# Kernel tuning notes

Hardware: AMD Instinct MI355X
Metric: run time of the kernel (lower is better)

The kernel has to match this reference:

```python
import jax, jax.numpy as jnp
import numpy as np

N, H, V, K = 2048, 1024, 50304, 16
C = V // K  # tokens per POS cluster


def setup_inputs() -> dict:
    key = jax.random.key(0)
    kx, ky, kw, kl = jax.random.split(key, 4)
    x = jax.random.normal(kx, (N, H), dtype=jnp.float32)
    y = jax.random.randint(ky, (N,), 0, V, dtype=jnp.int32)
    # consistent POS label: token y belongs to cluster y // C
    y_pos = (y // C).astype(jnp.int32)
    # pos2token[i] = token ids of cluster i (equal contiguous partition)
    pos2token = jnp.arange(V, dtype=jnp.int32).reshape(K, C)
    # token_in_pos_id[i][v] = within-cluster index of token v in cluster i
    token_in_pos_id = jnp.broadcast_to(jnp.arange(V, dtype=jnp.int32) % C, (K, V))
    cluster_w = jax.random.normal(kw, (H, K), dtype=jnp.float32) * 0.02
    logits = jax.random.normal(kl, (H, V), dtype=jnp.float32) * 0.02
    return {"x": x, "y": y, "y_pos": y_pos, "pos2token": pos2token,
            "token_in_pos_id": token_in_pos_id, "cluster_w": cluster_w, "logits": logits}


def reference(x, y, y_pos, pos2token, token_in_pos_id, cluster_w, logits):
    # cluster (POS) log-probs: [N, K]
    cluster_ll = jax.nn.log_softmax(x @ cluster_w, axis=1)
    # per-cluster weight slices gathered once: [H, K, C]
    W = logits[:, pos2token.reshape(-1)].reshape(H, K, C)
    # tail logits for every token against every cluster's token set: [N, K, C]
    tail_lp = jax.nn.log_softmax(jnp.einsum('nh,hkc->nkc', x, W), axis=-1)
    n = jnp.arange(y.shape[0])
    within = token_in_pos_id[y_pos, y]          # within-cluster target id
    nll = -cluster_ll[n, y_pos] - tail_lp[n, y_pos, within]
    return nll
```

## Files before the change

kernel.cpp:

```cpp
#include <hip/hip_runtime.h>
#include <hip/hip_bf16.h>

#define NROW 2048
#define HDIM 1024
#define VOC  50304
#define KCL  16
#define CDIM 3144

#define MT 128
#define NT 128
#define BK 32
#define CAP 256

#define WS_SUMEXP 0
#define WS_COUNTS 2048
#define WS_PART   2064
#define WS_ZTGT   4112
#define WS_TCOL   6160
#define WS_ROWS   8208
#define WS_XG     40976

typedef __attribute__((ext_vector_type(8))) short short8;
typedef __attribute__((ext_vector_type(4))) short short4v;
typedef __attribute__((ext_vector_type(4))) float f32x4;

__device__ __forceinline__ ushort2 f2bf2(float a, float b) {
    union { __hip_bfloat162 h; ushort2 u; } cv;
    cv.h = __float22bfloat162_rn(float2{a, b});
    return cv.u;
}

__device__ __forceinline__ void gload_lds16(const void* g, void* l) {
    const uint32_t __attribute__((address_space(1)))* gp =
        reinterpret_cast<const uint32_t __attribute__((address_space(1)))*>(
            reinterpret_cast<uintptr_t>(g));
    uint32_t __attribute__((address_space(3)))* lp =
        reinterpret_cast<uint32_t __attribute__((address_space(3)))*>(
            static_cast<uint32_t>(reinterpret_cast<uintptr_t>(l)));
    __builtin_amdgcn_global_load_lds(gp, lp, 16, 0, 0);
}

__global__ void scatter_kernel(const int* __restrict__ y,
                               const int* __restrict__ y_pos,
                               const int* __restrict__ tip,
                               int* ws_i) {
    int n = blockIdx.x * 256 + threadIdx.x;
    if (n >= NROW) return;
    int kn = y_pos[n];
    int slot = atomicAdd(&ws_i[WS_COUNTS + kn], 1);
    ws_i[WS_ROWS + kn * NROW + slot] = n;
    ws_i[WS_TCOL + n] = tip[kn * VOC + y[n]];
}

__global__ void prep_kernel(const float* __restrict__ x,
                            const float* __restrict__ cw,
                            const int* __restrict__ ws_i, float* ws_f) {
    const int wave = threadIdx.x >> 6;
    const int lane = threadIdx.x & 63;
    const int gw = blockIdx.x * 4 + wave;
    const int k = gw >> 8;
    const int slot = gw & (CAP - 1);
    const int Mk = ws_i[WS_COUNTS + k];
    short4v* dst = (short4v*)((const short*)(ws_i + WS_XG) + ((size_t)gw << 10));
    if (slot >= Mk) {
        short4v z = {0, 0, 0, 0};
#pragma unroll
        for (int q = 0; q < 4; q++) dst[q * 64 + lane] = z;
        return;
    }
    const int n = ws_i[WS_ROWS + k * NROW + slot];
    const float4* xr = (const float4*)(x + (size_t)n * HDIM);
    float4 v[4];
#pragma unroll
    for (int q = 0; q < 4; q++) v[q] = xr[q * 64 + lane];
#pragma unroll
    for (int q = 0; q < 4; q++) {
        union { ushort2 u2[2]; short4v s4; } t;
        t.u2[0] = f2bf2(v[q].x, v[q].y);
        t.u2[1] = f2bf2(v[q].z, v[q].w);
        dst[q * 64 + lane] = t.s4;
    }
    float acc[KCL];
#pragma unroll
    for (int kk = 0; kk < KCL; kk++) acc[kk] = 0.f;
#pragma unroll
    for (int q = 0; q < 4; q++) {
        const float* vf = (const float*)&v[q];
#pragma unroll
        for (int e = 0; e < 4; e++) {
            const int h = q * 256 + lane * 4 + e;
            const float xv = vf[e];
            const float4* cwr = (const float4*)(cw + (size_t)h * KCL);
#pragma unroll
            for (int qq = 0; qq < 4; qq++) {
                float4 w = cwr[qq];
                acc[qq * 4 + 0] += xv * w.x;
                acc[qq * 4 + 1] += xv * w.y;
                acc[qq * 4 + 2] += xv * w.z;
                acc[qq * 4 + 3] += xv * w.w;
            }
        }
    }
#pragma unroll
    for (int off = 32; off >= 1; off >>= 1) {
#pragma unroll
        for (int kk = 0; kk < KCL; kk++) acc[kk] += __shfl_down(acc[kk], off);
    }
    if (lane == 0) {
        float m = acc[0];
#pragma unroll
        for (int kk = 1; kk < KCL; kk++) m = fmaxf(m, acc[kk]);
        float s = 0.f;
#pragma unroll
        for (int kk = 0; kk < KCL; kk++) s += __expf(acc[kk] - m);
        ws_f[WS_PART + n] = (m + __logf(s)) - acc[k];
    }
}

__launch_bounds__(256, 2)
__global__ void tail_kernel(const float* __restrict__ logits,
                            const int* ws_i, float* ws_f) {
    __shared__ __align__(16) short As[4 * MT * 8];
    __shared__ __align__(16) short Bs[4 * NT * 8];
    __shared__ int   lrow[MT];
    __shared__ int   ltcol[MT];
    __shared__ float rowsum[MT];

    const int k  = blockIdx.y;
    const int ct = blockIdx.x;
    const int rt = blockIdx.z;
    const int Mk = ws_i[WS_COUNTS + k];
    if (rt * MT >= Mk) return;

    const int tid = threadIdx.x;
    if (tid < MT) {
        int r = rt * MT + tid;
        int rid = (r < Mk) ? ws_i[WS_ROWS + k * NROW + r] : -1;
        lrow[tid]  = rid;
        ltcol[tid] = (rid >= 0) ? ws_i[WS_TCOL + rid] : -1;
        rowsum[tid] = 0.f;
    }

    const short* xg = (const short*)(ws_i + WS_XG)
                    + ((size_t)(k * CAP + rt * MT) << 10);
    const int row0 = tid & 127;
    const int k80  = tid >> 7;
    const short* xrow = xg + (size_t)row0 * HDIM;

    const int w  = tid >> 6;
    const int l  = tid & 63;
    const int col0 = ct * NT + 2 * l;
    const int cp   = (col0 <= CDIM - 2) ? col0 : (CDIM - 2);
    const float* bp = logits + (size_t)(w * 8) * VOC + (k * CDIM + cp);

    const int wr   = (w >> 1) * 64;
    const int wc   = (w & 1) * 64;
    const int quad = l >> 4;
    const int lm   = l & 15;

    f32x4 acc[4][4];
#pragma unroll
    for (int mi = 0; mi < 4; mi++)
#pragma unroll
        for (int ni = 0; ni < 4; ni++) acc[mi][ni] = (f32x4)(0.f);

    __syncthreads();

    for (int h0 = 0; h0 < HDIM; h0 += BK) {
        gload_lds16(xrow + (k80 * 8) + h0,       &As[(size_t)tid * 8]);
        gload_lds16(xrow + ((k80 + 2) * 8) + h0, &As[(size_t)(256 + tid) * 8]);

        {
            float2 bv[8];
            const float* bpp = bp + (size_t)h0 * VOC;
#pragma unroll
            for (int j = 0; j < 8; j++)
                bv[j] = *(const float2*)(bpp + (size_t)j * VOC);
            union { ushort2 u2[4]; short8 s8; } ue, uo;
#pragma unroll
            for (int t = 0; t < 4; t++) {
                ue.u2[t] = f2bf2(bv[2 * t].x, bv[2 * t + 1].x);
                uo.u2[t] = f2bf2(bv[2 * t].y, bv[2 * t + 1].y);
            }
            *(short8*)&Bs[(size_t)(w * 128 + l) * 8]      = ue.s8;
            *(short8*)&Bs[(size_t)(w * 128 + 64 + l) * 8] = uo.s8;
        }
        __syncthreads();

        short8 a[4], b[4];
#pragma unroll
        for (int mi = 0; mi < 4; mi++)
            a[mi] = *(const short8*)&As[(size_t)(quad * 128 + wr + mi * 16 + lm) * 8];
#pragma unroll
        for (int ni = 0; ni < 4; ni++) {
            int C = wc + ni * 16 + lm;
            int cperm = (C >> 1) | ((C & 1) << 6);
            b[ni] = *(const short8*)&Bs[(size_t)(quad * 128 + cperm) * 8];
        }
#pragma unroll
        for (int mi = 0; mi < 4; mi++)
#pragma unroll
            for (int ni = 0; ni < 4; ni++)
                acc[mi][ni] = __builtin_amdgcn_mfma_f32_16x16x32_bf16(
                    a[mi], b[ni], acc[mi][ni], 0, 0, 0);
        __syncthreads();
    }

#pragma unroll
    for (int mi = 0; mi < 4; mi++) {
#pragma unroll
        for (int r = 0; r < 4; r++) {
            int row_local = wr + mi * 16 + quad * 4 + r;
            int rid = lrow[row_local];
            int tc  = ltcol[row_local];
            float s = 0.f;
#pragma unroll
            for (int ni = 0; ni < 4; ni++) {
                int cl = ct * NT + wc + ni * 16 + lm;
                float z = acc[mi][ni][r];
                if (rid >= 0 && cl < CDIM) {
                    s += __expf(z);
                    if (cl == tc) ws_f[WS_ZTGT + rid] = z;
                }
            }
            s += __shfl_xor(s, 1);
            s += __shfl_xor(s, 2);
            s += __shfl_xor(s, 4);
            s += __shfl_xor(s, 8);
            if (lm == 0 && rid >= 0) atomicAdd(&rowsum[row_local], s);
        }
    }
    __syncthreads();
    if (tid < MT) {
        int rid = lrow[tid];
        if (rid >= 0) atomicAdd(&ws_f[WS_SUMEXP + rid], rowsum[tid]);
    }
}

__global__ void finalize_kernel(const float* ws_f, float* __restrict__ out) {
    int n = blockIdx.x * 256 + threadIdx.x;
    if (n >= NROW) return;
    out[n] = ws_f[WS_PART + n] + __logf(ws_f[WS_SUMEXP + n]) - ws_f[WS_ZTGT + n];
}

extern "C" void kernel_launch(void* const* d_in, const int* in_sizes, int n_in,
                              void* d_out, int out_size, void* d_ws, size_t ws_size,
                              hipStream_t stream) {
    const float* x      = (const float*)d_in[0];
    const int*   y      = (const int*)d_in[1];
    const int*   y_pos  = (const int*)d_in[2];
    const int*   tip    = (const int*)d_in[4];
    const float* cw     = (const float*)d_in[5];
    const float* logits = (const float*)d_in[6];
    float* out  = (float*)d_out;
    float* ws_f = (float*)d_ws;
    int*   ws_i = (int*)d_ws;

    hipMemsetAsync(d_ws, 0, (size_t)(NROW + KCL) * 4, stream);

    scatter_kernel<<<NROW / 256, 256, 0, stream>>>(y, y_pos, tip, ws_i);
    prep_kernel<<<KCL * CAP / 4, 256, 0, stream>>>(x, cw, ws_i, ws_f);

    dim3 grid((CDIM + NT - 1) / NT, KCL, CAP / MT);
    tail_kernel<<<grid, 256, 0, stream>>>(logits, ws_i, ws_f);

    finalize_kernel<<<NROW / 256, 256, 0, stream>>>(ws_f, out);
}
```

Before: 383.8 us.

## Double-buffer tail GEMM, shrink column tile, and pre-transpose gathered x layout

The tail GEMM now double-buffers its A and B LDS tiles, issuing the next K-slice's global loads before the current MFMAs so load latency overlaps compute. The column tile drops from 128 to 64 with an occupancy hint of 4 blocks per CU. The prep kernel stages bf16 x rows in shared memory and writes them in an h-major blocked layout so tail loads are contiguous per K-step. The trade-off is more LDS per block, fewer MFMAs per B load, and B column reads that are now only 4-byte scalars.

```diff
diff --git a/kernel.cpp b/kernel.cpp
--- a/kernel.cpp
+++ b/kernel.cpp
@@ -8,9 +8,12 @@
 #define CDIM 3144
 
 #define MT 128
-#define NT 128
+#define NTC 64
 #define BK 32
 #define CAP 256
+
+#define ASZ (4 * 128 * 8)
+#define BSZ (4 * 64 * 8)
 
 #define WS_SUMEXP 0
 #define WS_COUNTS 2048
@@ -55,73 +58,87 @@
 __global__ void prep_kernel(const float* __restrict__ x,
                             const float* __restrict__ cw,
                             const int* __restrict__ ws_i, float* ws_f) {
-    const int wave = threadIdx.x >> 6;
+    __shared__ __align__(16) short rb[4][128][8];
+
+    const int wv   = threadIdx.x >> 6;
     const int lane = threadIdx.x & 63;
-    const int gw = blockIdx.x * 4 + wave;
-    const int k = gw >> 8;
-    const int slot = gw & (CAP - 1);
+    const int b = blockIdx.x;
+    const int k = b >> 6;
+    const int slot0 = (b & 63) * 4;
+    const int slot  = slot0 + wv;
     const int Mk = ws_i[WS_COUNTS + k];
-    short4v* dst = (short4v*)((const short*)(ws_i + WS_XG) + ((size_t)gw << 10));
-    if (slot >= Mk) {
-        short4v z = {0, 0, 0, 0};
-#pragma unroll
-        for (int q = 0; q < 4; q++) dst[q * 64 + lane] = z;
-        return;
-    }
-    const int n = ws_i[WS_ROWS + k * NROW + slot];
-    const float4* xr = (const float4*)(x + (size_t)n * HDIM);
+
     float4 v[4];
-#pragma unroll
-    for (int q = 0; q < 4; q++) v[q] = xr[q * 64 + lane];
+    if (slot < Mk) {
+        const int n = ws_i[WS_ROWS + k * NROW + slot];
+        const float4* xr = (const float4*)(x + (size_t)n * HDIM);
+#pragma unroll
+        for (int q = 0; q < 4; q++) v[q] = xr[q * 64 + lane];
+    } else {
+#pragma unroll
+        for (int q = 0; q < 4; q++) v[q] = float4{0.f, 0.f, 0.f, 0.f};
+    }
 #pragma unroll
     for (int q = 0; q < 4; q++) {
-        union { ushort2 u2[2]; short4v s4; } t;
+        union { ushort2 u2[2]; uint2 u; } t;
         t.u2[0] = f2bf2(v[q].x, v[q].y);
         t.u2[1] = f2bf2(v[q].z, v[q].w);
-        dst[q * 64 + lane] = t.s4;
-    }
-    float acc[KCL];
-#pragma unroll
-    for (int kk = 0; kk < KCL; kk++) acc[kk] = 0.f;
-#pragma unroll
-    for (int q = 0; q < 4; q++) {
-        const float* vf = (const float*)&v[q];
-#pragma unroll
-        for (int e = 0; e < 4; e++) {
-            const int h = q * 256 + lane * 4 + e;
-            const float xv = vf[e];
-            const float4* cwr = (const float4*)(cw + (size_t)h * KCL);
-#pragma unroll
-            for (int qq = 0; qq < 4; qq++) {
-                float4 w = cwr[qq];
-                acc[qq * 4 + 0] += xv * w.x;
-                acc[qq * 4 + 1] += xv * w.y;
-                acc[qq * 4 + 2] += xv * w.z;
-                acc[qq * 4 + 3] += xv * w.w;
+        *(uint2*)&rb[wv][q * 32 + (lane >> 1)][(lane & 1) * 4] = t.u;
+    }
+    if (slot < Mk) {
+        float acc[KCL];
+#pragma unroll
+        for (int kk = 0; kk < KCL; kk++) acc[kk] = 0.f;
+#pragma unroll
+        for (int q = 0; q < 4; q++) {
+            const float* vf = (const float*)&v[q];
+#pragma unroll
+            for (int e = 0; e < 4; e++) {
+                const int h = q * 256 + lane * 4 + e;
+                const float xv = vf[e];
+                const float4* cwr = (const float4*)(cw + (size_t)h * KCL);
+#pragma unroll
+                for (int qq = 0; qq < 4; qq++) {
+                    float4 wgt = cwr[qq];
+                    acc[qq * 4 + 0] += xv * wgt.x;
+                    acc[qq * 4 + 1] += xv * wgt.y;
+                    acc[qq * 4 + 2] += xv * wgt.z;
+                    acc[qq * 4 + 3] += xv * wgt.w;
+                }
             }
         }
-    }
-#pragma unroll
-    for (int off = 32; off >= 1; off >>= 1) {
-#pragma unroll
-        for (int kk = 0; kk < KCL; kk++) acc[kk] += __shfl_down(acc[kk], off);
-    }
-    if (lane == 0) {
-        float m = acc[0];
-#pragma unroll
-        for (int kk = 1; kk < KCL; kk++) m = fmaxf(m, acc[kk]);
-        float s = 0.f;
-#pragma unroll
-        for (int kk = 0; kk < KCL; kk++) s += __expf(acc[kk] - m);
-        ws_f[WS_PART + n] = (m + __logf(s)) - acc[k];
-    }
-}
-
-__launch_bounds__(256, 2)
+#pragma unroll
+        for (int off = 32; off >= 1; off >>= 1) {
+#pragma unroll
+            for (int kk = 0; kk < KCL; kk++) acc[kk] += __shfl_down(acc[kk], off);
+        }
+        if (lane == 0) {
+            const int n = ws_i[WS_ROWS + k * NROW + slot];
+            float m = acc[0];
+#pragma unroll
+            for (int kk = 1; kk < KCL; kk++) m = fmaxf(m, acc[kk]);
+            float s = 0.f;
+#pragma unroll
+            for (int kk = 0; kk < KCL; kk++) s += __expf(acc[kk] - m);
+            ws_f[WS_PART + n] = (m + __logf(s)) - acc[k];
+        }
+    }
+    __syncthreads();
+    {
+        const int h8 = threadIdx.x >> 1;
+        const int sp = (threadIdx.x & 1) * 2;
+        short* o = (short*)(ws_i + WS_XG)
+                 + ((size_t)k * (128 * 256) + (size_t)h8 * 256 + slot0 + sp) * 8;
+        *(short8*)(o)     = *(const short8*)&rb[sp][h8][0];
+        *(short8*)(o + 8) = *(const short8*)&rb[sp + 1][h8][0];
+    }
+}
+
+__launch_bounds__(256, 4)
 __global__ void tail_kernel(const float* __restrict__ logits,
                             const int* ws_i, float* ws_f) {
-    __shared__ __align__(16) short As[4 * MT * 8];
-    __shared__ __align__(16) short Bs[4 * NT * 8];
+    __shared__ __align__(16) short As[2 * ASZ];
+    __shared__ __align__(16) short Bs[2 * BSZ];
     __shared__ int   lrow[MT];
     __shared__ int   ltcol[MT];
     __shared__ float rowsum[MT];
@@ -141,68 +158,77 @@
         rowsum[tid] = 0.f;
     }
 
-    const short* xg = (const short*)(ws_i + WS_XG)
-                    + ((size_t)(k * CAP + rt * MT) << 10);
+    const short* xgT = (const short*)(ws_i + WS_XG);
     const int row0 = tid & 127;
     const int k80  = tid >> 7;
-    const short* xrow = xg + (size_t)row0 * HDIM;
-
-    const int w  = tid >> 6;
-    const int l  = tid & 63;
-    const int col0 = ct * NT + 2 * l;
-    const int cp   = (col0 <= CDIM - 2) ? col0 : (CDIM - 2);
-    const float* bp = logits + (size_t)(w * 8) * VOC + (k * CDIM + cp);
-
-    const int wr   = (w >> 1) * 64;
-    const int wc   = (w & 1) * 64;
-    const int quad = l >> 4;
-    const int lm   = l & 15;
-
-    f32x4 acc[4][4];
+    const short* aSrc0 = xgT + ((size_t)k * (128 * 256)
+                              + (size_t)(k80 * 256 + rt * MT + row0)) * 8;
+    const short* aSrc1 = aSrc0 + 2 * 256 * 8;
+
+    const int c  = tid & 63;
+    const int kg = tid >> 6;
+    const int col0 = ct * NTC + c;
+    const int cp = (col0 < CDIM) ? col0 : (CDIM - 1);
+    const float* bSrc = logits + (size_t)(kg * 8) * VOC + ((size_t)k * CDIM + cp);
+
+    const int w  = tid >> 6, l = tid & 63;
+    const int wr = (w & 1) * 64;
+    const int wc = (w >> 1) * 32;
+    const int quad = l >> 4, lm = l & 15;
+
+    f32x4 acc[4][2];
 #pragma unroll
     for (int mi = 0; mi < 4; mi++)
 #pragma unroll
-        for (int ni = 0; ni < 4; ni++) acc[mi][ni] = (f32x4)(0.f);
-
+        for (int ni = 0; ni < 2; ni++) acc[mi][ni] = (f32x4)(0.f);
+
+    gload_lds16(aSrc0, As + tid * 8);
+    gload_lds16(aSrc1, As + (256 + tid) * 8);
+    {
+        float bv[8];
+#pragma unroll
+        for (int j = 0; j < 8; j++) bv[j] = bSrc[(size_t)j * VOC];
+        union { ushort2 u2[4]; short8 s8; } u;
+#pragma unroll
+        for (int jj = 0; jj < 4; jj++) u.u2[jj] = f2bf2(bv[2 * jj], bv[2 * jj + 1]);
+        *(short8*)(Bs + (kg * 64 + c) * 8) = u.s8;
+    }
     __syncthreads();
 
-    for (int h0 = 0; h0 < HDIM; h0 += BK) {
-        gload_lds16(xrow + (k80 * 8) + h0,       &As[(size_t)tid * 8]);
-        gload_lds16(xrow + ((k80 + 2) * 8) + h0, &As[(size_t)(256 + tid) * 8]);
-
-        {
-            float2 bv[8];
-            const float* bpp = bp + (size_t)h0 * VOC;
+    for (int t = 0; t < HDIM / BK; ++t) {
+        const int cur = t & 1;
+        short* asb = As + cur * ASZ;
+        short* bsb = Bs + cur * BSZ;
+        float bv[8];
+        const bool pf = (t < HDIM / BK - 1);
+        if (pf) {
+            short* asn = As + (cur ^ 1) * ASZ;
+            gload_lds16(aSrc0 + (size_t)(t + 1) * 8192, asn + tid * 8);
+            gload_lds16(aSrc1 + (size_t)(t + 1) * 8192, asn + (256 + tid) * 8);
 #pragma unroll
             for (int j = 0; j < 8; j++)
-                bv[j] = *(const float2*)(bpp + (size_t)j * VOC);
-            union { ushort2 u2[4]; short8 s8; } ue, uo;
-#pragma unroll
-            for (int t = 0; t < 4; t++) {
-                ue.u2[t] = f2bf2(bv[2 * t].x, bv[2 * t + 1].x);
-                uo.u2[t] = f2bf2(bv[2 * t].y, bv[2 * t + 1].y);
-            }
-            *(short8*)&Bs[(size_t)(w * 128 + l) * 8]      = ue.s8;
-            *(short8*)&Bs[(size_t)(w * 128 + 64 + l) * 8] = uo.s8;
-        }
-        __syncthreads();
-
-        short8 a[4], b[4];
+                bv[j] = bSrc[(size_t)((t + 1) * BK + j) * VOC];
+        }
+        short8 a[4], b[2];
 #pragma unroll
         for (int mi = 0; mi < 4; mi++)
-            a[mi] = *(const short8*)&As[(size_t)(quad * 128 + wr + mi * 16 + lm) * 8];
-#pragma unroll
-        for (int ni = 0; ni < 4; ni++) {
-            int C = wc + ni * 16 + lm;
-            int cperm = (C >> 1) | ((C & 1) << 6);
-            b[ni] = *(const short8*)&Bs[(size_t)(quad * 128 + cperm) * 8];
-        }
+            a[mi] = *(const short8*)(asb + (quad * 128 + wr + mi * 16 + lm) * 8);
+#pragma unroll
+        for (int ni = 0; ni < 2; ni++)
+            b[ni] = *(const short8*)(bsb + (quad * 64 + wc + ni * 16 + lm) * 8);
 #pragma unroll
         for (int mi = 0; mi < 4; mi++)
 #pragma unroll
-            for (int ni = 0; ni < 4; ni++)
+            for (int ni = 0; ni < 2; ni++)
                 acc[mi][ni] = __builtin_amdgcn_mfma_f32_16x16x32_bf16(
                     a[mi], b[ni], acc[mi][ni], 0, 0, 0);
+        if (pf) {
+            short* bsn = Bs + (cur ^ 1) * BSZ;
+            union { ushort2 u2[4]; short8 s8; } u;
+#pragma unroll
+            for (int jj = 0; jj < 4; jj++) u.u2[jj] = f2bf2(bv[2 * jj], bv[2 * jj + 1]);
+            *(short8*)(bsn + (kg * 64 + c) * 8) = u.s8;
+        }
         __syncthreads();
     }
 
@@ -215,8 +241,8 @@
             int tc  = ltcol[row_local];
             float s = 0.f;
 #pragma unroll
-            for (int ni = 0; ni < 4; ni++) {
-                int cl = ct * NT + wc + ni * 16 + lm;
+            for (int ni = 0; ni < 2; ni++) {
+                int cl = ct * NTC + wc + ni * 16 + lm;
                 float z = acc[mi][ni][r];
                 if (rid >= 0 && cl < CDIM) {
                     s += __expf(z);
@@ -261,7 +287,7 @@
     scatter_kernel<<<NROW / 256, 256, 0, stream>>>(y, y_pos, tip, ws_i);
     prep_kernel<<<KCL * CAP / 4, 256, 0, stream>>>(x, cw, ws_i, ws_f);
 
-    dim3 grid((CDIM + NT - 1) / NT, KCL, CAP / MT);
+    dim3 grid((CDIM + NTC - 1) / NTC, KCL, CAP / MT);
     tail_kernel<<<grid, 256, 0, stream>>>(logits, ws_i, ws_f);
 
     finalize_kernel<<<NROW / 256, 256, 0, stream>>>(ws_f, out);
```

Result: faster. 366.0 us (-4.6%).
